# Kernel optimization log

Measured on AMD Instinct MI355X. Metric: run time of the kernel, lower is better.

Reference implementation:

```python
import jax, jax.numpy as jnp
import numpy as np

SEQ, BATCH = 1024, 2
N_HEAD, D_MODEL = 16, 1024
Q_LORA, KV_LORA = 20, 20
ROPE = D_MODEL // N_HEAD // 2   # 32 qk_rope_head_dim
NOPE = D_MODEL // N_HEAD // 2   # 32 qk_nope_head_dim
V_DIM = D_MODEL // N_HEAD       # 64
N_EXP, HID = 4, 1024            # hidden_dim = d_inner//5 = 5120//5
N_GROUP, TOPK_GROUP, TOP_K = 2, 2, 1
ROUTED_SCALE = 1.0


def setup_inputs() -> dict:
    key = jax.random.key(0)
    ks = jax.random.split(key, 16)
    sc = 0.02
    return {
        'dec_inp': jax.random.normal(ks[0], (SEQ, BATCH, D_MODEL), jnp.float32),
        'wq_a': jax.random.normal(ks[1], (D_MODEL, Q_LORA), jnp.float32) * sc,
        'q_norm_w': jnp.ones((Q_LORA,), jnp.float32),
        'wq_b': jax.random.normal(ks[2], (Q_LORA, N_HEAD * (NOPE + ROPE)), jnp.float32) * sc,
        'wkv_a': jax.random.normal(ks[3], (D_MODEL, KV_LORA + ROPE), jnp.float32) * sc,
        'kv_norm_w': jnp.ones((KV_LORA,), jnp.float32),
        'wkv_b': jax.random.normal(ks[4], (KV_LORA, N_HEAD * (NOPE + V_DIM)), jnp.float32) * sc,
        'wo': jax.random.normal(ks[5], (N_HEAD * V_DIM, D_MODEL), jnp.float32) * sc,
        'gate_w': jax.random.normal(ks[6], (N_EXP, D_MODEL), jnp.float32) * sc,
        'exp_gate': jax.random.normal(ks[7], (N_EXP, D_MODEL, HID), jnp.float32) * sc,
        'exp_up': jax.random.normal(ks[8], (N_EXP, D_MODEL, HID), jnp.float32) * sc,
        'exp_down': jax.random.normal(ks[9], (N_EXP, HID, D_MODEL), jnp.float32) * sc,
        'sh_gate': jax.random.normal(ks[10], (D_MODEL, HID), jnp.float32) * sc,
        'sh_up': jax.random.normal(ks[11], (D_MODEL, HID), jnp.float32) * sc,
        'sh_down': jax.random.normal(ks[12], (HID, D_MODEL), jnp.float32) * sc,
    }


def _rms(x, w, eps=1e-6):
    return x * jax.lax.rsqrt(jnp.mean(x * x, axis=-1, keepdims=True) + eps) * w


def _freqs(seqlen):
    # precompute_freqs_cis(rope_dim * n_head, seqlen): dim = 512 here
    dim = ROPE * N_HEAD
    inv = 1.0 / (10000.0 ** (jnp.arange(0, dim, 2, dtype=jnp.float32) / dim))  # [dim//2]
    ang = jnp.arange(seqlen, dtype=jnp.float32)[:, None] * inv[None, :]       # [s, dim//2]
    ang = ang.reshape(seqlen, N_HEAD, ROPE // 2)
    return jnp.cos(ang), jnp.sin(ang)


def _rope(x, cos, sin):
    # x: [b, s, h, ROPE]; interleaved-pair complex rotation
    b, s, h, _ = x.shape
    xr = x.reshape(b, s, h, ROPE // 2, 2)
    x0, x1 = xr[..., 0], xr[..., 1]
    c = cos[None]  # [1, s, h, ROPE//2]
    sn = sin[None]
    o0 = x0 * c - x1 * sn
    o1 = x0 * sn + x1 * c
    return jnp.stack([o0, o1], axis=-1).reshape(b, s, h, ROPE)


def reference(dec_inp, wq_a, q_norm_w, wq_b, wkv_a, kv_norm_w, wkv_b, wo,
              gate_w, exp_gate, exp_up, exp_down, sh_gate, sh_up, sh_down):
    x = jnp.swapaxes(dec_inp, 0, 1)  # [b, s, d]
    b, s, d = x.shape
    # ---- MLA attention ----
    q = _rms(x @ wq_a, q_norm_w) @ wq_b                       # [b, s, h*(nope+rope)]
    q = q.reshape(b, s, N_HEAD, NOPE + ROPE)
    q_nope, q_pe = q[..., :NOPE], q[..., NOPE:]
    kv = x @ wkv_a                                            # [b, s, kv_lora+rope]
    ckv, k_pe = kv[..., :KV_LORA], kv[..., KV_LORA:]
    kvb = (_rms(ckv, kv_norm_w) @ wkv_b).reshape(b, s, N_HEAD, NOPE + V_DIM)
    k_nope, v = kvb[..., :NOPE], kvb[..., NOPE:]
    cos, sin = _freqs(s)
    q_pe = _rope(q_pe, cos, sin)
    k_pe_h = _rope(jnp.broadcast_to(k_pe[:, :, None, :], (b, s, N_HEAD, ROPE)), cos, sin)
    qf = jnp.concatenate([q_nope, q_pe], axis=-1)             # [b, s, h, 64]
    kf = jnp.concatenate([k_nope, k_pe_h], axis=-1)
    scale = 1.0 / np.sqrt(NOPE + ROPE)
    scores = jnp.einsum('bshd,bthd->bhst', qf, kf) * scale    # mask=None in the source forward
    probs = jax.nn.softmax(scores, axis=-1)
    attn = jnp.einsum('bhst,bthd->bshd', probs, v).reshape(b, s, N_HEAD * V_DIM)
    y = attn @ wo                                             # [b, s, d]
    y = jnp.swapaxes(y, 0, 1)                                 # [s, b, d]
    # ---- DeepSeekMoE (group_limited_greedy, top_k=1, 1 shared expert) ----
    xf = y.reshape(-1, d)                                     # [T, d]
    T = xf.shape[0]
    sc = jax.nn.softmax(xf @ gate_w.T, axis=-1)               # [T, E]
    gsc = sc.reshape(T, N_GROUP, N_EXP // N_GROUP).max(axis=-1)  # [T, n_group]
    _, gidx = jax.lax.top_k(gsc, TOPK_GROUP)
    gmask = jax.nn.one_hot(gidx, N_GROUP, dtype=sc.dtype).sum(axis=1)  # [T, n_group]
    smask = jnp.repeat(gmask, N_EXP // N_GROUP, axis=-1)      # [T, E]
    tw, ti = jax.lax.top_k(jnp.where(smask > 0, sc, 0.0), TOP_K)
    comb = (jax.nn.one_hot(ti, N_EXP, dtype=sc.dtype) * tw[..., None]).sum(axis=1) * ROUTED_SCALE  # [T, E]
    g = jnp.einsum('td,edh->teh', xf, exp_gate)
    u = jnp.einsum('td,edh->teh', xf, exp_up)
    dn = jnp.einsum('teh,ehd->ted', jax.nn.silu(g) * u, exp_down)
    routed = jnp.einsum('ted,te->td', dn, comb)
    shared = (jax.nn.silu(xf @ sh_gate) * (xf @ sh_up)) @ sh_down
    return (routed + shared).reshape(s, b, d)
```

## Files before the change

### kernel.cpp

```cpp
#include <hip/hip_runtime.h>
#include <hip/hip_bf16.h>
#include <math.h>

#define SEQ 1024
#define BATCH 2
#define T 2048
#define DM 1024
#define NH 16
#define NOPE 32
#define HD 64
#define QL 20
#define KVL 20
#define KVA 52
#define HID 1024
#define NEXP 4
#define LSTR 80

typedef short bf16x8 __attribute__((ext_vector_type(8)));
typedef float f32x4 __attribute__((ext_vector_type(4)));
typedef float f32x16 __attribute__((ext_vector_type(16)));
typedef __hip_bfloat16 bf16;

static __device__ __forceinline__ float sigmoidf_(float x) {
    return 1.0f / (1.0f + __expf(-x));
}
static __device__ __forceinline__ unsigned short bfbits(float x) {
    bf16 h = __float2bfloat16(x);
    return *reinterpret_cast<unsigned short*>(&h);
}
static __device__ __forceinline__ unsigned cvt_pk_bf16(float lo, float hi) {
    unsigned r;
    asm("v_cvt_pk_bf16_f32 %0, %1, %2" : "=v"(r) : "v"(lo), "v"(hi));
    return r;
}
static __device__ __forceinline__ void gload16(const bf16* g, char* l) {
    __builtin_amdgcn_global_load_lds(
        (const __attribute__((address_space(1))) unsigned int*)g,
        (__attribute__((address_space(3))) unsigned int*)l, 16, 0, 0);
}
static __device__ __forceinline__ void barrier_() {
    asm volatile("" ::: "memory");
    __builtin_amdgcn_s_barrier();
    asm volatile("" ::: "memory");
}
#define VMWAIT(N) asm volatile("s_waitcnt vmcnt(" #N ")" ::: "memory")

__global__ __launch_bounds__(256) void k_setup(
    const float* __restrict__ wo, const float* __restrict__ sg,
    const float* __restrict__ su, const float* __restrict__ sd,
    const float* __restrict__ eg, const float* __restrict__ eu,
    const float* __restrict__ ed,
    bf16* __restrict__ woT, bf16* __restrict__ sgT, bf16* __restrict__ suT,
    bf16* __restrict__ sdT, bf16* __restrict__ egT, bf16* __restrict__ euT,
    bf16* __restrict__ edT,
    const float* __restrict__ wq_a, const float* __restrict__ wkv_a,
    const float* __restrict__ wq_b, const float* __restrict__ wkv_b,
    bf16* __restrict__ loraT, bf16* __restrict__ wqbT, bf16* __restrict__ wkvbT,
    float* __restrict__ ctab, float* __restrict__ stab)
{
    int z = blockIdx.z;
    int tid = threadIdx.x;
    if (z < 16) {
        __shared__ float tile[32][33];
        const float* in; bf16* out;
        if      (z == 0) { in = wo; out = woT; }
        else if (z == 1) { in = sg; out = sgT; }
        else if (z == 2) { in = su; out = suT; }
        else if (z == 3) { in = sd; out = sdT; }
        else if (z < 8)  { size_t o = (size_t)(z - 4)  * DM * HID; in = eg + o; out = egT + o; }
        else if (z < 12) { size_t o = (size_t)(z - 8)  * DM * HID; in = eu + o; out = euT + o; }
        else             { size_t o = (size_t)(z - 12) * HID * DM; in = ed + o; out = edT + o; }
        int c0 = blockIdx.x * 32, r0 = blockIdx.y * 32;
        int tx = tid & 31, ty = tid >> 5;
        #pragma unroll
        for (int ii = 0; ii < 4; ++ii)
            tile[ty + ii * 8][tx] = in[(size_t)(r0 + ty + ii * 8) * 1024 + c0 + tx];
        __syncthreads();
        int c = tid >> 3, rg = (tid & 7) * 4;
        ushort4 o4;
        o4.x = bfbits(tile[rg + 0][c]);
        o4.y = bfbits(tile[rg + 1][c]);
        o4.z = bfbits(tile[rg + 2][c]);
        o4.w = bfbits(tile[rg + 3][c]);
        *(ushort4*)&out[(size_t)(c0 + c) * 1024 + r0 + rg] = o4;
    } else if (z == 16) {
        int s = blockIdx.y * 32 + blockIdx.x;
        int p = tid;
        float freq = exp2f(-(float)p * (13.287712379549449f / 256.0f));
        float ang = (float)s * freq;
        float sn, cs;
        __sincosf(ang, &sn, &cs);
        ctab[s * 256 + p] = cs;
        stab[s * 256 + p] = sn;
    } else {
        int idx = (blockIdx.y * 32 + blockIdx.x) * 256 + tid;
        if (z == 17) {
            if (idx >= 80 * 1024) return;
            int n = idx >> 10, k = idx & 1023;
            float v = (n < 20) ? wq_a[k * QL + n] : (n < 72 ? wkv_a[k * KVA + (n - 20)] : 0.f);
            loraT[idx] = __float2bfloat16(v);
        } else if (z == 18) {
            if (idx >= 1024 * 32) return;
            int n = idx >> 5, k = idx & 31;
            wqbT[idx] = __float2bfloat16(k < 20 ? wq_b[k * DM + n] : 0.f);
        } else {
            if (idx >= 1536 * 32) return;
            int n = idx >> 5, k = idx & 31;
            wkvbT[idx] = __float2bfloat16(k < 20 ? wkv_b[k * (NH * 96) + n] : 0.f);
        }
    }
}

__global__ __launch_bounds__(256) void k_p1(
    const float* __restrict__ dec, const bf16* __restrict__ loraT,
    float* __restrict__ lora4)
{
    __shared__ __align__(16) char As[128 * LSTR];
    __shared__ __align__(16) char Bs[80 * LSTR];
    const int tid = threadIdx.x;
    const int kz = blockIdx.x;
    const int m0 = blockIdx.y * 128;
    const int lane = tid & 63, wave = tid >> 6;
    const int g = lane >> 4, c = lane & 15;
    f32x4 acc[2][5] = {};
    for (int ks = 0; ks < 16; ++ks) {
        int k0 = kz * 512 + ks * 32;
        __syncthreads();
        #pragma unroll
        for (int pass = 0; pass < 4; ++pass) {
            int row = (tid >> 3) + pass * 32;
            int t = m0 + row;
            int b = t >> 10, s = t & 1023;
            f32x4 v = *(const f32x4*)&dec[(size_t)(s * 2 + b) * DM + k0 + (tid & 7) * 4];
            ushort4 h4;
            h4.x = bfbits(v[0]); h4.y = bfbits(v[1]);
            h4.z = bfbits(v[2]); h4.w = bfbits(v[3]);
            *(ushort4*)&As[row * LSTR + (tid & 7) * 8] = h4;
        }
        if (tid < 160) {
            int row = tid >> 1, hf = tid & 1;
            const bf16* src = &loraT[row * 1024 + k0 + hf * 16];
            *(int4*)&Bs[row * LSTR + hf * 32]      = *(const int4*)&src[0];
            *(int4*)&Bs[row * LSTR + hf * 32 + 16] = *(const int4*)&src[8];
        }
        __syncthreads();
        bf16x8 af[2], bff[5];
        #pragma unroll
        for (int mi = 0; mi < 2; ++mi)
            af[mi] = *(const bf16x8*)&As[(wave * 32 + mi * 16 + c) * LSTR + 16 * g];
        #pragma unroll
        for (int nf = 0; nf < 5; ++nf)
            bff[nf] = *(const bf16x8*)&Bs[(nf * 16 + c) * LSTR + 16 * g];
        #pragma unroll
        for (int mi = 0; mi < 2; ++mi)
            #pragma unroll
            for (int nf = 0; nf < 5; ++nf)
                acc[mi][nf] = __builtin_amdgcn_mfma_f32_16x16x32_bf16(af[mi], bff[nf], acc[mi][nf], 0, 0, 0);
    }
    #pragma unroll
    for (int mi = 0; mi < 2; ++mi)
        #pragma unroll
        for (int nf = 0; nf < 5; ++nf)
            #pragma unroll
            for (int r = 0; r < 4; ++r) {
                int col = nf * 16 + c;
                if (col < 72) {
                    int row = m0 + wave * 32 + mi * 16 + 4 * g + r;
                    lora4[((size_t)kz * T + row) * 72 + col] = acc[mi][nf][r];
                }
            }
}

__global__ __launch_bounds__(256) void k_p2m(
    const float* __restrict__ lora4, const float* __restrict__ qnw,
    const float* __restrict__ kvnw, const float* __restrict__ ctab,
    const float* __restrict__ stab, bf16* __restrict__ nrmq,
    bf16* __restrict__ nrmkv, bf16* __restrict__ kb, int* __restrict__ cnt)
{
    int bid = blockIdx.x, tid = threadIdx.x;
    if (bid == 0 && tid < 16) cnt[tid] = 0;
    {
        int t = bid, p = tid;
        int r = p & 15, h = p >> 4, s = t & (SEQ - 1);
        float y0 = lora4[t * 72 + 40 + 2 * r] + lora4[(size_t)(T + t) * 72 + 40 + 2 * r];
        float y1 = lora4[t * 72 + 41 + 2 * r] + lora4[(size_t)(T + t) * 72 + 41 + 2 * r];
        float cs = ctab[s * 256 + p], sn = stab[s * 256 + p];
        ushort2 pk;
        pk.x = bfbits(y0 * cs - y1 * sn);
        pk.y = bfbits(y0 * sn + y1 * cs);
        *(ushort2*)&kb[(size_t)t * DM + h * HD + NOPE + 2 * r] = pk;
    }
    if (bid < 8) {
        int t = bid * 256 + tid;
        float lq[20], lk[20];
        float ssq = 0.f, ssk = 0.f;
        #pragma unroll
        for (int i = 0; i < 20; ++i) {
            lq[i] = lora4[t * 72 + i] + lora4[(size_t)(T + t) * 72 + i];
            ssq += lq[i] * lq[i];
        }
        #pragma unroll
        for (int i = 0; i < 20; ++i) {
            lk[i] = lora4[t * 72 + 20 + i] + lora4[(size_t)(T + t) * 72 + 20 + i];
            ssk += lk[i] * lk[i];
        }
        float fq = rsqrtf(ssq / 20.f + 1e-6f);
        float fk = rsqrtf(ssk / 20.f + 1e-6f);
        #pragma unroll
        for (int i = 0; i < 32; ++i) {
            nrmq[t * 32 + i]  = __float2bfloat16(i < 20 ? lq[i] * fq * qnw[i]  : 0.f);
            nrmkv[t * 32 + i] = __float2bfloat16(i < 20 ? lk[i] * fk * kvnw[i] : 0.f);
        }
    }
}

__global__ __launch_bounds__(256) void k_p3(
    const bf16* __restrict__ nrmq, const bf16* __restrict__ wqbT,
    const bf16* __restrict__ nrmkv, const bf16* __restrict__ wkvbT,
    const float* __restrict__ ctab, const float* __restrict__ stab,
    bf16* __restrict__ qb, bf16* __restrict__ kb, bf16* __restrict__ vt_g)
{
    const int zq = (blockIdx.z == 0);
    if (zq && blockIdx.x >= 16) return;
    __shared__ __align__(16) char As[128 * LSTR];
    __shared__ __align__(16) char Bs[64 * LSTR];
    const int tid = threadIdx.x;
    const int m0 = blockIdx.y * 128, n0 = blockIdx.x * 64;
    const int lane = tid & 63, wave = tid >> 6;
    const int g = lane >> 4, c = lane & 15;
    const int wm = wave >> 1, wn = wave & 1;
    const bf16* nrm = zq ? nrmq : nrmkv;
    const bf16* wT  = zq ? wqbT : wkvbT;
    {
        int row = tid >> 1, hf = tid & 1;
        const bf16* sa = &nrm[(size_t)(m0 + row) * 32 + hf * 16];
        *(int4*)&As[row * LSTR + hf * 32]      = *(const int4*)&sa[0];
        *(int4*)&As[row * LSTR + hf * 32 + 16] = *(const int4*)&sa[8];
        int brow = tid >> 2;
        *(int4*)&Bs[brow * LSTR + (tid & 3) * 16] = *(const int4*)&wT[(size_t)(n0 + brow) * 32 + (tid & 3) * 8];
    }
    __syncthreads();
    f32x4 acc[4][2] = {};
    bf16x8 af[4], bfr[2];
    #pragma unroll
    for (int mi = 0; mi < 4; ++mi)
        af[mi] = *(const bf16x8*)&As[(wm * 64 + mi * 16 + c) * LSTR + 16 * g];
    #pragma unroll
    for (int ni = 0; ni < 2; ++ni)
        bfr[ni] = *(const bf16x8*)&Bs[(wn * 32 + ni * 16 + c) * LSTR + 16 * g];
    #pragma unroll
    for (int mi = 0; mi < 4; ++mi)
        #pragma unroll
        for (int ni = 0; ni < 2; ++ni)
            acc[mi][ni] = __builtin_amdgcn_mfma_f32_16x16x32_bf16(af[mi], bfr[ni], acc[mi][ni], 0, 0, 0);

    if (zq) {
        #pragma unroll
        for (int mi = 0; mi < 4; ++mi)
            #pragma unroll
            for (int ni = 0; ni < 2; ++ni) {
                #pragma unroll
                for (int r = 0; r < 4; ++r) acc[mi][ni][r] *= 0.18033688f;
                int n = n0 + wn * 32 + ni * 16 + c;
                int w = n & 63;
                if (w < 32) {
                    #pragma unroll
                    for (int r = 0; r < 4; ++r) {
                        int row = m0 + wm * 64 + mi * 16 + 4 * g + r;
                        qb[(size_t)row * DM + n] = __float2bfloat16(acc[mi][ni][r]);
                    }
                } else {
                    int h = n >> 6;
                    int pidx = h * 16 + ((w - 32) >> 1);
                    int odd = w & 1;
                    #pragma unroll
                    for (int r = 0; r < 4; ++r) {
                        int row = m0 + wm * 64 + mi * 16 + 4 * g + r;
                        int s = row & (SEQ - 1);
                        float own = acc[mi][ni][r];
                        float oth = __shfl_xor(own, 1);
                        float cs = ctab[s * 256 + pidx], sn = stab[s * 256 + pidx];
                        float o = odd ? (oth * sn + own * cs) : (own * cs - oth * sn);
                        qb[(size_t)row * DM + n] = __float2bfloat16(o);
                    }
                }
            }
    } else {
        #pragma unroll
        for (int mi = 0; mi < 4; ++mi)
            #pragma unroll
            for (int ni = 0; ni < 2; ++ni) {
                int n = n0 + wn * 32 + ni * 16 + c;
                int h = n / 96, w = n - h * 96;
                int row0 = m0 + wm * 64 + mi * 16 + 4 * g;
                if (w < NOPE) {
                    #pragma unroll
                    for (int r = 0; r < 4; ++r)
                        kb[(size_t)(row0 + r) * DM + h * HD + w] = __float2bfloat16(acc[mi][ni][r]);
                } else {
                    int d = w - NOPE;
                    int b = row0 >> 10, s0 = row0 & (SEQ - 1);
                    ushort4 v4;
                    v4.x = bfbits(acc[mi][ni][0]);
                    v4.y = bfbits(acc[mi][ni][1]);
                    v4.z = bfbits(acc[mi][ni][2]);
                    v4.w = bfbits(acc[mi][ni][3]);
                    *(ushort4*)&vt_g[(((size_t)(b * NH + h) * HD + d) << 10) + s0] = v4;
                }
            }
    }
}

__global__ __launch_bounds__(256) void k_attn(
    const bf16* __restrict__ qb, const bf16* __restrict__ kb,
    const bf16* __restrict__ vt_g, bf16* __restrict__ ab)
{
    __shared__ __align__(16) char stage[2][16384];

    const int orig = blockIdx.y * 8 + blockIdx.x;
    const int h  = (orig & 7) * 2 + ((orig >> 3) & 1);
    const int qt = orig >> 4;
    const int b = blockIdx.z;
    const int tid = threadIdx.x;
    const int lane = tid & 63, wave = tid >> 6;
    const int l31 = lane & 31, hi = lane >> 5;
    const int sp = wave >> 1, wq = wave & 1;
    const int q0 = qt * 64 + wq * 32;
    char* ks = stage[sp];
    char* vt = stage[sp] + 8192;

    const int scol = ((lane & 7) * 8) ^ ((lane >> 3) << 3);
    const int srowL = lane >> 3;

    bf16x8 qf[4];
    {
        const bf16* qrow = &qb[(size_t)(b * SEQ + q0 + l31) * DM + h * HD + 8 * hi];
        #pragma unroll
        for (int st = 0; st < 4; ++st)
            qf[st] = *(const bf16x8*)&qrow[16 * st];
    }

    f32x16 o0 = {}, o1 = {};
    float m_run = -3.0e38f, l_run = 0.f;
    const size_t vbase = ((size_t)(b * NH + h) * HD) << 10;

    for (int ktl = 0; ktl < 8; ++ktl) {
        const int kt = sp * 8 + ktl;
        __syncthreads();
        #pragma unroll
        for (int ps = 0; ps < 4; ++ps) {
            int rbase = ps * 16 + wq * 8;
            int row = rbase + srowL;
            gload16(&kb[(size_t)(b * SEQ + kt * 64 + row) * DM + h * HD + scol],
                    ks + rbase * 128);
            gload16(&vt_g[vbase + ((size_t)row << 10) + kt * 64 + scol],
                    vt + rbase * 128);
        }
        VMWAIT(0);
        __syncthreads();

        f32x16 sc0 = {}, sc1 = {};
        __builtin_amdgcn_s_setprio(1);
        #pragma unroll
        for (int st = 0; st < 4; ++st) {
            int colb = 32 * st + 16 * hi;
            int r0 = l31;
            bf16x8 kf0 = *(const bf16x8*)&ks[r0 * 128 + (colb ^ ((r0 & 7) << 4))];
            sc0 = __builtin_amdgcn_mfma_f32_32x32x16_bf16(kf0, qf[st], sc0, 0, 0, 0);
            int r1 = 32 + l31;
            bf16x8 kf1 = *(const bf16x8*)&ks[r1 * 128 + (colb ^ ((r1 & 7) << 4))];
            sc1 = __builtin_amdgcn_mfma_f32_32x32x16_bf16(kf1, qf[st], sc1, 0, 0, 0);
        }
        __builtin_amdgcn_s_setprio(0);

        float mt = fmaxf(sc0[0], sc1[0]);
        #pragma unroll
        for (int i = 1; i < 16; ++i) mt = fmaxf(mt, fmaxf(sc0[i], sc1[i]));
        mt = fmaxf(mt, __shfl_xor(mt, 32));

        if (!__all(mt <= m_run + 8.0f)) {
            float m_new = fmaxf(m_run, mt);
            float corr = exp2f(m_run - m_new);
            m_run = m_new;
            l_run *= corr;
            #pragma unroll
            for (int i = 0; i < 16; ++i) { o0[i] *= corr; o1[i] *= corr; }
        }
        float ls = 0.f;
        #pragma unroll
        for (int i = 0; i < 16; ++i) {
            sc0[i] = exp2f(sc0[i] - m_run);
            sc1[i] = exp2f(sc1[i] - m_run);
            ls += sc0[i] + sc1[i];
        }
        ls += __shfl_xor(ls, 32);
        l_run += ls;

        unsigned pk0[8], pk1[8];
        #pragma unroll
        for (int i = 0; i < 8; ++i) {
            pk0[i] = cvt_pk_bf16(sc0[2 * i], sc0[2 * i + 1]);
            pk1[i] = cvt_pk_bf16(sc1[2 * i], sc1[2 * i + 1]);
        }

        __builtin_amdgcn_s_setprio(1);
#define PV_SUB(PK, KK)                                                          \
        {                                                                       \
            _Pragma("unroll")                                                   \
            for (int s = 0; s < 2; ++s) {                                       \
                unsigned sx = hi ? PK[4*s]   : PK[4*s+2];                       \
                unsigned rx = __shfl_xor(sx, 32);                               \
                unsigned sy = hi ? PK[4*s+1] : PK[4*s+3];                       \
                unsigned ry = __shfl_xor(sy, 32);                               \
                int4 bi;                                                        \
                bi.x = hi ? (int)rx : (int)PK[4*s];                             \
                bi.y = hi ? (int)ry : (int)PK[4*s+1];                           \
                bi.z = hi ? (int)PK[4*s+2] : (int)rx;                           \
                bi.w = hi ? (int)PK[4*s+3] : (int)ry;                           \
                bf16x8 bfr = *(bf16x8*)&bi;                                     \
                int cb = (KK) * 64 + 32 * s + 16 * hi;                          \
                {                                                               \
                    int vr = l31;                                               \
                    bf16x8 vf = *(const bf16x8*)&vt[vr * 128 + (cb ^ ((vr & 7) << 4))]; \
                    o0 = __builtin_amdgcn_mfma_f32_32x32x16_bf16(vf, bfr, o0, 0, 0, 0); \
                }                                                               \
                {                                                               \
                    int vr = 32 + l31;                                          \
                    bf16x8 vf = *(const bf16x8*)&vt[vr * 128 + (cb ^ ((vr & 7) << 4))]; \
                    o1 = __builtin_amdgcn_mfma_f32_32x32x16_bf16(vf, bfr, o1, 0, 0, 0); \
                }                                                               \
            }                                                                   \
        }
        PV_SUB(pk0, 0)
        PV_SUB(pk1, 1)
#undef PV_SUB
        __builtin_amdgcn_s_setprio(0);
    }

    float* polB = (float*)stage[0];
    float* mllB = (float*)(stage[0] + 16640 - 16384 + 16384);
    mllB = (float*)(stage[0] + 16640);

    __syncthreads();
    if (sp == 1) {
        #pragma unroll
        for (int i = 0; i < 16; ++i) {
            int d = (i & 3) + 8 * (i >> 2) + 4 * hi;
            polB[(wq * 32 + l31) * 65 + d]      = o0[i];
            polB[(wq * 32 + l31) * 65 + 32 + d] = o1[i];
        }
        if (hi == 0) {
            mllB[(wq * 32 + l31) * 2 + 0] = m_run;
            mllB[(wq * 32 + l31) * 2 + 1] = l_run;
        }
    }
    __syncthreads();
    if (sp == 0) {
        float m_b = mllB[(wq * 32 + l31) * 2 + 0];
        float l_b = mllB[(wq * 32 + l31) * 2 + 1];
        float M = fmaxf(m_run, m_b);
        float wa = exp2f(m_run - M), wb = exp2f(m_b - M);
        float inv = 1.0f / (l_run * wa + l_b * wb);
        #pragma unroll
        for (int i = 0; i < 16; ++i) {
            int d = (i & 3) + 8 * (i >> 2) + 4 * hi;
            o0[i] = (o0[i] * wa + polB[(wq * 32 + l31) * 65 + d]      * wb) * inv;
            o1[i] = (o1[i] * wa + polB[(wq * 32 + l31) * 65 + 32 + d] * wb) * inv;
        }
    }
    __syncthreads();
    if (sp == 0) {
        char* tb = stage[1] + 1024 + wq * 8192 / 2 * 0 + wq * 7168;
        tb = stage[1] + (wq ? 8192 : 1024);
        #pragma unroll
        for (int i = 0; i < 8; ++i) {
            int dbase = 2 * (i & 1) + 8 * (i >> 1) + 4 * hi;
            *(unsigned*)&tb[l31 * 140 + (dbase) * 2]      = cvt_pk_bf16(o0[2 * i], o0[2 * i + 1]);
            *(unsigned*)&tb[l31 * 140 + (32 + dbase) * 2] = cvt_pk_bf16(o1[2 * i], o1[2 * i + 1]);
        }
        __builtin_amdgcn_s_waitcnt(0);
        #pragma unroll
        for (int p = 0; p < 8; ++p) {
            int idx = p * 64 + lane;
            int q = idx >> 4, c8 = idx & 15;
            int2 rv;
            rv.x = *(const int*)&tb[q * 140 + c8 * 8];
            rv.y = *(const int*)&tb[q * 140 + c8 * 8 + 4];
            *(int2*)&ab[(size_t)(b * SEQ + q0 + q) * DM + h * HD + c8 * 4] = rv;
        }
    }
}

__global__ __launch_bounds__(512) void k_mm_plain(
    const bf16* __restrict__ A, const bf16* __restrict__ Bt, bf16* __restrict__ C)
{
    __shared__ __align__(16) char As[3][8192];
    __shared__ __align__(16) char Bs[3][4096];
    const int tid = threadIdx.x;
    const int lane = tid & 63, wave = tid >> 6;
    const int g = lane >> 4, c = lane & 15;
    const int wm = wave >> 1, wn = wave & 1;
    int orig = blockIdx.y * 16 + blockIdx.x;
    int swz = (orig & 7) * 32 + (orig >> 3);
    const int n0 = (swz & 15) * 64, m0 = (swz >> 4) * 128;

    const int ldr = lane >> 2;
    const int ldc = (lane & 3) * 8;
    const bf16* agp = &A[(size_t)(m0 + wave * 16 + ldr) * DM + ldc];
    const bool doB = wave >= 4;
    const bf16* bgp = &Bt[(size_t)(n0 + (wave & 3) * 16 + ldr) * DM + ldc];
    const int aoffL = wave * 1024, boffL = (wave & 3) * 1024;

    f32x4 acc[2][2] = {};
    const int NT = DM / 32;
    gload16(agp, As[0] + aoffL);
    if (doB) gload16(bgp, Bs[0] + boffL);
    int cur = 0;
    for (int k = 0; k < NT; ++k) {
        if (k + 1 < NT) {
            int nxt = (cur + 1) % 3;
            gload16(agp + (k + 1) * 32, As[nxt] + aoffL);
            if (doB) gload16(bgp + (k + 1) * 32, Bs[nxt] + boffL);
            if (doB) VMWAIT(2); else VMWAIT(1);
        } else {
            VMWAIT(0);
        }
        barrier_();
        bf16x8 af[2], bfx[2];
        #pragma unroll
        for (int mi = 0; mi < 2; ++mi)
            af[mi] = *(const bf16x8*)&As[cur][(wm * 32 + mi * 16 + c) * 64 + g * 16];
        #pragma unroll
        for (int ni = 0; ni < 2; ++ni)
            bfx[ni] = *(const bf16x8*)&Bs[cur][(wn * 32 + ni * 16 + c) * 64 + g * 16];
        #pragma unroll
        for (int mi = 0; mi < 2; ++mi)
            #pragma unroll
            for (int ni = 0; ni < 2; ++ni)
                acc[mi][ni] = __builtin_amdgcn_mfma_f32_16x16x32_bf16(af[mi], bfx[ni], acc[mi][ni], 0, 0, 0);
        cur = (cur + 1) % 3;
    }
    #pragma unroll
    for (int mi = 0; mi < 2; ++mi)
        #pragma unroll
        for (int ni = 0; ni < 2; ++ni)
            #pragma unroll
            for (int r = 0; r < 4; ++r)
                C[(size_t)(m0 + wm * 32 + mi * 16 + 4 * g + r) * DM + n0 + wn * 32 + ni * 16 + c]
                    = __float2bfloat16(acc[mi][ni][r]);
}

__global__ __launch_bounds__(512) void k_mm_gu_all(
    const bf16* __restrict__ X, const bf16* __restrict__ egT,
    const bf16* __restrict__ euT, const bf16* __restrict__ sgT,
    const bf16* __restrict__ suT, const int* __restrict__ cnt,
    const int* __restrict__ lists, bf16* __restrict__ act_r,
    bf16* __restrict__ act_s)
{
    const int e = blockIdx.z;
    const bool SH = (e == 4);
    const int ntok = SH ? T : cnt[e];
    int orig = blockIdx.y * 16 + blockIdx.x;
    int swz = (orig & 7) * 32 + (orig >> 3);
    const int n0 = (swz & 15) * 64, m0 = (swz >> 4) * 128;
    if (m0 >= ntok) return;
    __shared__ __align__(16) char As[3][8192];
    __shared__ __align__(16) char Bg[3][4096];
    __shared__ __align__(16) char Bu[3][4096];
    __shared__ int rowid[128];
    const int tid = threadIdx.x;
    if (tid < 128) {
        int idx = m0 + tid;
        rowid[tid] = SH ? idx : lists[e * T + (idx < ntok ? idx : ntok - 1)];
    }
    __syncthreads();
    const int lane = tid & 63, wave = tid >> 6;
    const int g = lane >> 4, c = lane & 15;
    const int wm = wave >> 1, wn = wave & 1;
    const bf16* Bge = SH ? sgT : egT + (size_t)e * HID * DM;
    const bf16* Bue = SH ? suT : euT + (size_t)e * HID * DM;
    bf16* act = SH ? act_s : act_r;

    const int ldr = lane >> 2;
    const int ldc = (lane & 3) * 8;
    const int myTok = rowid[wave * 16 + ldr];
    const bf16* agp = &X[(size_t)myTok * DM + ldc];
    const bool isG = wave < 4;
    const bf16* bgp = (isG ? Bge : Bue) + (size_t)(n0 + (wave & 3) * 16 + ldr) * DM + ldc;
    const int aoffL = wave * 1024, boffL = (wave & 3) * 1024;

    f32x4 accg[2][2] = {}, accu[2][2] = {};
    const int NT = DM / 32;
    gload16(agp, As[0] + aoffL);
    gload16(bgp, (isG ? Bg[0] : Bu[0]) + boffL);
    int cur = 0;
    for (int k = 0; k < NT; ++k) {
        if (k + 1 < NT) {
            int nxt = (cur + 1) % 3;
            gload16(agp + (k + 1) * 32, As[nxt] + aoffL);
            gload16(bgp + (k + 1) * 32, (isG ? Bg[nxt] : Bu[nxt]) + boffL);
            VMWAIT(2);
        } else {
            VMWAIT(0);
        }
        barrier_();
        bf16x8 af[2], gf[2], uf[2];
        #pragma unroll
        for (int mi = 0; mi < 2; ++mi)
            af[mi] = *(const bf16x8*)&As[cur][(wm * 32 + mi * 16 + c) * 64 + g * 16];
        #pragma unroll
        for (int ni = 0; ni < 2; ++ni) {
            gf[ni] = *(const bf16x8*)&Bg[cur][(wn * 32 + ni * 16 + c) * 64 + g * 16];
            uf[ni] = *(const bf16x8*)&Bu[cur][(wn * 32 + ni * 16 + c) * 64 + g * 16];
        }
        #pragma unroll
        for (int mi = 0; mi < 2; ++mi)
            #pragma unroll
            for (int ni = 0; ni < 2; ++ni) {
                accg[mi][ni] = __builtin_amdgcn_mfma_f32_16x16x32_bf16(af[mi], gf[ni], accg[mi][ni], 0, 0, 0);
                accu[mi][ni] = __builtin_amdgcn_mfma_f32_16x16x32_bf16(af[mi], uf[ni], accu[mi][ni], 0, 0, 0);
            }
        cur = (cur + 1) % 3;
    }
    #pragma unroll
    for (int mi = 0; mi < 2; ++mi)
        #pragma unroll
        for (int ni = 0; ni < 2; ++ni)
            #pragma unroll
            for (int r = 0; r < 4; ++r) {
                int lr = wm * 32 + mi * 16 + 4 * g + r;
                if (!SH && m0 + lr >= ntok) continue;
                int token = rowid[lr];
                float gv = accg[mi][ni][r], uv = accu[mi][ni][r];
                act[(size_t)token * HID + n0 + wn * 32 + ni * 16 + c] =
                    __float2bfloat16(gv * sigmoidf_(gv) * uv);
            }
}

__global__ __launch_bounds__(512) void k_mm_down_f(
    const bf16* __restrict__ Xr, const bf16* __restrict__ Xs,
    const bf16* __restrict__ edT, const bf16* __restrict__ sdT,
    const int* __restrict__ cnt, const int* __restrict__ lists,
    const float* __restrict__ wtok, float* __restrict__ out)
{
    const int e = blockIdx.z;
    const int ntok = cnt[e];
    int orig = blockIdx.y * 16 + blockIdx.x;
    int swz = (orig & 7) * 32 + (orig >> 3);
    const int n0 = (swz & 15) * 64, m0 = (swz >> 4) * 128;
    if (m0 >= ntok) return;
    __shared__ __align__(16) char Ar[3][8192];
    __shared__ __align__(16) char Az[3][8192];
    __shared__ __align__(16) char Br[3][4096];
    __shared__ __align__(16) char Bz[3][4096];
    __shared__ int rowid[128];
    const int tid = threadIdx.x;
    if (tid < 128) {
        int idx = m0 + tid;
        rowid[tid] = lists[e * T + (idx < ntok ? idx : ntok - 1)];
    }
    __syncthreads();
    const int lane = tid & 63, wave = tid >> 6;
    const int g = lane >> 4, c = lane & 15;
    const int wm = wave >> 1, wn = wave & 1;
    const bf16* Bde = edT + (size_t)e * HID * DM;

    const int ldr = lane >> 2;
    const int ldc = (lane & 3) * 8;
    const int myTok = rowid[wave * 16 + ldr];
    const bf16* agr = &Xr[(size_t)myTok * HID + ldc];
    const bf16* ags = &Xs[(size_t)myTok * HID + ldc];
    const bool isR = wave < 4;
    const bf16* bgp = (isR ? Bde : sdT) + (size_t)(n0 + (wave & 3) * 16 + ldr) * HID + ldc;
    const int aoffL = wave * 1024, boffL = (wave & 3) * 1024;

    f32x4 accr[2][2] = {}, accs[2][2] = {};
    const int NT = HID / 32;
    gload16(agr, Ar[0] + aoffL);
    gload16(ags, Az[0] + aoffL);
    gload16(bgp, (isR ? Br[0] : Bz[0]) + boffL);
    int cur = 0;
    for (int k = 0; k < NT; ++k) {
        if (k + 1 < NT) {
            int nxt = (cur + 1) % 3;
            gload16(agr + (k + 1) * 32, Ar[nxt] + aoffL);
            gload16(ags + (k + 1) * 32, Az[nxt] + aoffL);
            gload16(bgp + (k + 1) * 32, (isR ? Br[nxt] : Bz[nxt]) + boffL);
            VMWAIT(3);
        } else {
            VMWAIT(0);
        }
        barrier_();
        bf16x8 afr[2], afs[2], bfr[2], bfs[2];
        #pragma unroll
        for (int mi = 0; mi < 2; ++mi) {
            afr[mi] = *(const bf16x8*)&Ar[cur][(wm * 32 + mi * 16 + c) * 64 + g * 16];
            afs[mi] = *(const bf16x8*)&Az[cur][(wm * 32 + mi * 16 + c) * 64 + g * 16];
        }
        #pragma unroll
        for (int ni = 0; ni < 2; ++ni) {
            bfr[ni] = *(const bf16x8*)&Br[cur][(wn * 32 + ni * 16 + c) * 64 + g * 16];
            bfs[ni] = *(const bf16x8*)&Bz[cur][(wn * 32 + ni * 16 + c) * 64 + g * 16];
        }
        #pragma unroll
        for (int mi = 0; mi < 2; ++mi)
            #pragma unroll
            for (int ni = 0; ni < 2; ++ni) {
                accr[mi][ni] = __builtin_amdgcn_mfma_f32_16x16x32_bf16(afr[mi], bfr[ni], accr[mi][ni], 0, 0, 0);
                accs[mi][ni] = __builtin_amdgcn_mfma_f32_16x16x32_bf16(afs[mi], bfs[ni], accs[mi][ni], 0, 0, 0);
            }
        cur = (cur + 1) % 3;
    }
    #pragma unroll
    for (int mi = 0; mi < 2; ++mi)
        #pragma unroll
        for (int ni = 0; ni < 2; ++ni)
            #pragma unroll
            for (int r = 0; r < 4; ++r) {
                int lr = wm * 32 + mi * 16 + 4 * g + r;
                if (m0 + lr >= ntok) continue;
                int token = rowid[lr];
                int bt = token >> 10, st = token & (SEQ - 1);
                size_t oo = (size_t)st * (BATCH * DM) + bt * DM + n0 + wn * 32 + ni * 16 + c;
                out[oo] = accr[mi][ni][r] * wtok[token] + accs[mi][ni][r];
            }
}

__global__ __launch_bounds__(256) void k_gate(
    const bf16* __restrict__ y, const float* __restrict__ gw,
    int* __restrict__ cnt, int* __restrict__ lists, float* __restrict__ wtok)
{
    int warp = threadIdx.x >> 6, lane = threadIdx.x & 63;
    int t = blockIdx.x * 4 + warp;
    float acc[NEXP] = {};
    for (int d = lane; d < DM; d += 64) {
        float xv = __bfloat162float(y[(size_t)t * DM + d]);
        #pragma unroll
        for (int e = 0; e < NEXP; ++e) acc[e] += xv * gw[e * DM + d];
    }
    #pragma unroll
    for (int off = 32; off; off >>= 1)
        #pragma unroll
        for (int e = 0; e < NEXP; ++e) acc[e] += __shfl_xor(acc[e], off);
    if (lane == 0) {
        float mx = fmaxf(fmaxf(acc[0], acc[1]), fmaxf(acc[2], acc[3]));
        float ex[NEXP], ssum = 0.f;
        #pragma unroll
        for (int e = 0; e < NEXP; ++e) { ex[e] = __expf(acc[e] - mx); ssum += ex[e]; }
        int best = 0; float bv = ex[0];
        #pragma unroll
        for (int e = 1; e < NEXP; ++e) if (ex[e] > bv) { bv = ex[e]; best = e; }
        wtok[t] = bv / ssum;
        int pos = atomicAdd(&cnt[best], 1);
        lists[best * T + pos] = t;
    }
}

extern "C" void kernel_launch(void* const* d_in, const int* in_sizes, int n_in,
                              void* d_out, int out_size, void* d_ws, size_t ws_size,
                              hipStream_t stream) {
    (void)in_sizes; (void)n_in; (void)out_size; (void)ws_size;
    const float* dec      = (const float*)d_in[0];
    const float* wq_a     = (const float*)d_in[1];
    const float* q_norm_w = (const float*)d_in[2];
    const float* wq_b     = (const float*)d_in[3];
    const float* wkv_a    = (const float*)d_in[4];
    const float* kv_norm_w= (const float*)d_in[5];
    const float* wkv_b    = (const float*)d_in[6];
    const float* wo       = (const float*)d_in[7];
    const float* gate_w   = (const float*)d_in[8];
    const float* exp_gate = (const float*)d_in[9];
    const float* exp_up   = (const float*)d_in[10];
    const float* exp_down = (const float*)d_in[11];
    const float* sh_gate  = (const float*)d_in[12];
    const float* sh_up    = (const float*)d_in[13];
    const float* sh_down  = (const float*)d_in[14];
    float* out = (float*)d_out;

    char* W = (char*)d_ws;
    bf16* qb   = (bf16*)(W);
    bf16* kb   = (bf16*)(W + (4ull  << 20));
    bf16* vt_g = (bf16*)(W + (8ull  << 20));
    char* SMALL = W + (12ull << 20);
    bf16* ab   = (bf16*)(W + (12ull << 20));
    bf16* woT = (bf16*)(W + (16ull << 20));
    bf16* sgT = (bf16*)(W + (18ull << 20));
    bf16* suT = (bf16*)(W + (20ull << 20));
    bf16* sdT = (bf16*)(W + (22ull << 20));
    bf16* egT = (bf16*)(W + (24ull << 20));
    bf16* euT = (bf16*)(W + (32ull << 20));
    bf16* edT = (bf16*)(W + (40ull << 20));
    int*   cnt   = (int*)(W + (48ull << 20));
    int*   lists = cnt + 16;
    float* wtok  = (float*)(lists + NEXP * T);
    bf16* yb    = qb;
    bf16* act_r = kb;
    bf16* act_s = vt_g;

    float* lora4 = (float*)(SMALL);
    bf16*  loraT = (bf16*) (SMALL + 1179648);
    bf16*  wqbT  = (bf16*) (SMALL + 1343488);
    bf16*  wkvbT = (bf16*) (SMALL + 1409024);
    bf16*  nrmq  = (bf16*) (SMALL + 1507328);
    bf16*  nrmkv = (bf16*) (SMALL + 1638400);
    float* ctab  = (float*)(SMALL + 1769472);
    float* stab  = (float*)(SMALL + 2818048);

    k_setup<<<dim3(32, 32, 20), 256, 0, stream>>>(
        wo, sh_gate, sh_up, sh_down, exp_gate, exp_up, exp_down,
        woT, sgT, suT, sdT, egT, euT, edT,
        wq_a, wkv_a, wq_b, wkv_b, loraT, wqbT, wkvbT, ctab, stab);

    k_p1<<<dim3(2, 16), 256, 0, stream>>>(dec, loraT, lora4);
    k_p2m<<<T, 256, 0, stream>>>(lora4, q_norm_w, kv_norm_w, ctab, stab,
                                 nrmq, nrmkv, kb, cnt);
    k_p3<<<dim3(24, 16, 2), 256, 0, stream>>>(nrmq, wqbT, nrmkv, wkvbT,
                                              ctab, stab, qb, kb, vt_g);

    k_attn<<<dim3(8, 32, BATCH), 256, 0, stream>>>(qb, kb, vt_g, ab);
    k_mm_plain<<<dim3(16, 16), 512, 0, stream>>>(ab, woT, yb);
    k_gate<<<T / 4, 256, 0, stream>>>(yb, gate_w, cnt, lists, wtok);
    k_mm_gu_all<<<dim3(16, 16, NEXP + 1), 512, 0, stream>>>(
        yb, egT, euT, sgT, suT, cnt, lists, act_r, act_s);
    k_mm_down_f<<<dim3(16, 16, NEXP), 512, 0, stream>>>(
        act_r, act_s, edT, sdT, cnt, lists, wtok, out);
}
```

Before: 172.5 us.

## Fuse FFN weight transpose/bf16 conversion into MoE GEMM B-tile loads

Drops the setup pass that transposed and converted all expert and shared FFN weights to bf16. The gate/up and down GEMM kernels now load fp32 weights directly into registers, convert them to bf16 and write them transposed into LDS, with a two-stage prefetch and LGKM wait plus barrier. This removes a large extra read and write of about 60MB of weights per call. In exchange, the main GEMM loops read fp32 (twice the bytes) through ordinary loads and do scalar 2-byte LDS stores.

```diff
diff --git a/kernel.cpp b/kernel.cpp
--- a/kernel.cpp
+++ b/kernel.cpp
@@ -44,15 +44,10 @@
     asm volatile("" ::: "memory");
 }
 #define VMWAIT(N) asm volatile("s_waitcnt vmcnt(" #N ")" ::: "memory")
+#define LGKM0()   asm volatile("s_waitcnt lgkmcnt(0)" ::: "memory")
 
 __global__ __launch_bounds__(256) void k_setup(
-    const float* __restrict__ wo, const float* __restrict__ sg,
-    const float* __restrict__ su, const float* __restrict__ sd,
-    const float* __restrict__ eg, const float* __restrict__ eu,
-    const float* __restrict__ ed,
-    bf16* __restrict__ woT, bf16* __restrict__ sgT, bf16* __restrict__ suT,
-    bf16* __restrict__ sdT, bf16* __restrict__ egT, bf16* __restrict__ euT,
-    bf16* __restrict__ edT,
+    const float* __restrict__ wo, bf16* __restrict__ woT,
     const float* __restrict__ wq_a, const float* __restrict__ wkv_a,
     const float* __restrict__ wq_b, const float* __restrict__ wkv_b,
     bf16* __restrict__ loraT, bf16* __restrict__ wqbT, bf16* __restrict__ wkvbT,
@@ -60,21 +55,13 @@
 {
     int z = blockIdx.z;
     int tid = threadIdx.x;
-    if (z < 16) {
+    if (z == 0) {
         __shared__ float tile[32][33];
-        const float* in; bf16* out;
-        if      (z == 0) { in = wo; out = woT; }
-        else if (z == 1) { in = sg; out = sgT; }
-        else if (z == 2) { in = su; out = suT; }
-        else if (z == 3) { in = sd; out = sdT; }
-        else if (z < 8)  { size_t o = (size_t)(z - 4)  * DM * HID; in = eg + o; out = egT + o; }
-        else if (z < 12) { size_t o = (size_t)(z - 8)  * DM * HID; in = eu + o; out = euT + o; }
-        else             { size_t o = (size_t)(z - 12) * HID * DM; in = ed + o; out = edT + o; }
         int c0 = blockIdx.x * 32, r0 = blockIdx.y * 32;
         int tx = tid & 31, ty = tid >> 5;
         #pragma unroll
         for (int ii = 0; ii < 4; ++ii)
-            tile[ty + ii * 8][tx] = in[(size_t)(r0 + ty + ii * 8) * 1024 + c0 + tx];
+            tile[ty + ii * 8][tx] = wo[(size_t)(r0 + ty + ii * 8) * 1024 + c0 + tx];
         __syncthreads();
         int c = tid >> 3, rg = (tid & 7) * 4;
         ushort4 o4;
@@ -82,8 +69,8 @@
         o4.y = bfbits(tile[rg + 1][c]);
         o4.z = bfbits(tile[rg + 2][c]);
         o4.w = bfbits(tile[rg + 3][c]);
-        *(ushort4*)&out[(size_t)(c0 + c) * 1024 + r0 + rg] = o4;
-    } else if (z == 16) {
+        *(ushort4*)&woT[(size_t)(c0 + c) * 1024 + r0 + rg] = o4;
+    } else if (z == 1) {
         int s = blockIdx.y * 32 + blockIdx.x;
         int p = tid;
         float freq = exp2f(-(float)p * (13.287712379549449f / 256.0f));
@@ -94,12 +81,12 @@
         stab[s * 256 + p] = sn;
     } else {
         int idx = (blockIdx.y * 32 + blockIdx.x) * 256 + tid;
-        if (z == 17) {
+        if (z == 2) {
             if (idx >= 80 * 1024) return;
             int n = idx >> 10, k = idx & 1023;
             float v = (n < 20) ? wq_a[k * QL + n] : (n < 72 ? wkv_a[k * KVA + (n - 20)] : 0.f);
             loraT[idx] = __float2bfloat16(v);
-        } else if (z == 18) {
+        } else if (z == 3) {
             if (idx >= 1024 * 32) return;
             int n = idx >> 5, k = idx & 31;
             wqbT[idx] = __float2bfloat16(k < 20 ? wq_b[k * DM + n] : 0.f);
@@ -438,8 +425,7 @@
     }
 
     float* polB = (float*)stage[0];
-    float* mllB = (float*)(stage[0] + 16640 - 16384 + 16384);
-    mllB = (float*)(stage[0] + 16640);
+    float* mllB = (float*)(stage[0] + 16640);
 
     __syncthreads();
     if (sp == 1) {
@@ -470,8 +456,7 @@
     }
     __syncthreads();
     if (sp == 0) {
-        char* tb = stage[1] + 1024 + wq * 8192 / 2 * 0 + wq * 7168;
-        tb = stage[1] + (wq ? 8192 : 1024);
+        char* tb = stage[1] + (wq ? 8192 : 1024);
         #pragma unroll
         for (int i = 0; i < 8; ++i) {
             int dbase = 2 * (i & 1) + 8 * (i >> 1) + 4 * hi;
@@ -551,9 +536,9 @@
 }
 
 __global__ __launch_bounds__(512) void k_mm_gu_all(
-    const bf16* __restrict__ X, const bf16* __restrict__ egT,
-    const bf16* __restrict__ euT, const bf16* __restrict__ sgT,
-    const bf16* __restrict__ suT, const int* __restrict__ cnt,
+    const bf16* __restrict__ X, const float* __restrict__ eg,
+    const float* __restrict__ eu, const float* __restrict__ sg,
+    const float* __restrict__ su, const int* __restrict__ cnt,
     const int* __restrict__ lists, bf16* __restrict__ act_r,
     bf16* __restrict__ act_s)
 {
@@ -577,8 +562,8 @@
     const int lane = tid & 63, wave = tid >> 6;
     const int g = lane >> 4, c = lane & 15;
     const int wm = wave >> 1, wn = wave & 1;
-    const bf16* Bge = SH ? sgT : egT + (size_t)e * HID * DM;
-    const bf16* Bue = SH ? suT : euT + (size_t)e * HID * DM;
+    const float* Wg = SH ? sg : eg + (size_t)e * DM * HID;
+    const float* Wu = SH ? su : eu + (size_t)e * DM * HID;
     bf16* act = SH ? act_s : act_r;
 
     const int ldr = lane >> 2;
@@ -586,24 +571,48 @@
     const int myTok = rowid[wave * 16 + ldr];
     const bf16* agp = &X[(size_t)myTok * DM + ldc];
     const bool isG = wave < 4;
-    const bf16* bgp = (isG ? Bge : Bue) + (size_t)(n0 + (wave & 3) * 16 + ldr) * DM + ldc;
-    const int aoffL = wave * 1024, boffL = (wave & 3) * 1024;
-
+    const int w4 = wave & 3, nb0 = w4 * 16;
+    const int ng = lane & 3, kk = lane >> 2;
+    const float* bq = (isG ? Wg : Wu) + (size_t)kk * HID + n0 + nb0 + ng * 4;
+    const int aoffL = wave * 1024;
+
+#define BWRITE(BUF)                                                             \
+    {                                                                           \
+        char* bb = (isG ? Bg[BUF] : Bu[BUF]);                                   \
+        _Pragma("unroll")                                                       \
+        for (int j = 0; j < 4; ++j) {                                           \
+            *(unsigned short*)&bb[(nb0 + ng * 4 + j) * 64 + kk * 2]        = bfbits(b0[j]); \
+            *(unsigned short*)&bb[(nb0 + ng * 4 + j) * 64 + (kk + 16) * 2] = bfbits(b1[j]); \
+        }                                                                       \
+    }
+
+    f32x4 b0, b1;
     f32x4 accg[2][2] = {}, accu[2][2] = {};
     const int NT = DM / 32;
+    b0 = *(const f32x4*)(bq);
+    b1 = *(const f32x4*)(bq + 16 * HID);
     gload16(agp, As[0] + aoffL);
-    gload16(bgp, (isG ? Bg[0] : Bu[0]) + boffL);
+    VMWAIT(1);
+    BWRITE(0)
+    b0 = *(const f32x4*)(bq + 32 * HID);
+    b1 = *(const f32x4*)(bq + 48 * HID);
+    gload16(agp + 32, As[1] + aoffL);
+    LGKM0();
+    barrier_();
     int cur = 0;
     for (int k = 0; k < NT; ++k) {
         if (k + 1 < NT) {
             int nxt = (cur + 1) % 3;
-            gload16(agp + (k + 1) * 32, As[nxt] + aoffL);
-            gload16(bgp + (k + 1) * 32, (isG ? Bg[nxt] : Bu[nxt]) + boffL);
-            VMWAIT(2);
+            VMWAIT(1);
+            BWRITE(nxt)
+            if (k + 2 < NT) {
+                b0 = *(const f32x4*)(bq + (size_t)(k + 2) * 32 * HID);
+                b1 = *(const f32x4*)(bq + (size_t)(k + 2) * 32 * HID + 16 * HID);
+                gload16(agp + (k + 2) * 32, As[(nxt + 1) % 3] + aoffL);
+            }
         } else {
             VMWAIT(0);
         }
-        barrier_();
         bf16x8 af[2], gf[2], uf[2];
         #pragma unroll
         for (int mi = 0; mi < 2; ++mi)
@@ -620,8 +629,11 @@
                 accg[mi][ni] = __builtin_amdgcn_mfma_f32_16x16x32_bf16(af[mi], gf[ni], accg[mi][ni], 0, 0, 0);
                 accu[mi][ni] = __builtin_amdgcn_mfma_f32_16x16x32_bf16(af[mi], uf[ni], accu[mi][ni], 0, 0, 0);
             }
+        LGKM0();
+        barrier_();
         cur = (cur + 1) % 3;
     }
+#undef BWRITE
     #pragma unroll
     for (int mi = 0; mi < 2; ++mi)
         #pragma unroll
@@ -639,7 +651,7 @@
 
 __global__ __launch_bounds__(512) void k_mm_down_f(
     const bf16* __restrict__ Xr, const bf16* __restrict__ Xs,
-    const bf16* __restrict__ edT, const bf16* __restrict__ sdT,
+    const float* __restrict__ ed, const float* __restrict__ sd,
     const int* __restrict__ cnt, const int* __restrict__ lists,
     const float* __restrict__ wtok, float* __restrict__ out)
 {
@@ -663,7 +675,6 @@
     const int lane = tid & 63, wave = tid >> 6;
     const int g = lane >> 4, c = lane & 15;
     const int wm = wave >> 1, wn = wave & 1;
-    const bf16* Bde = edT + (size_t)e * HID * DM;
 
     const int ldr = lane >> 2;
     const int ldc = (lane & 3) * 8;
@@ -671,26 +682,52 @@
     const bf16* agr = &Xr[(size_t)myTok * HID + ldc];
     const bf16* ags = &Xs[(size_t)myTok * HID + ldc];
     const bool isR = wave < 4;
-    const bf16* bgp = (isR ? Bde : sdT) + (size_t)(n0 + (wave & 3) * 16 + ldr) * HID + ldc;
-    const int aoffL = wave * 1024, boffL = (wave & 3) * 1024;
-
+    const int w4 = wave & 3, nb0 = w4 * 16;
+    const int ng = lane & 3, kk = lane >> 2;
+    const float* bq = (isR ? (ed + (size_t)e * HID * DM) : sd)
+                      + (size_t)kk * DM + n0 + nb0 + ng * 4;
+    const int aoffL = wave * 1024;
+
+#define BWRITE(BUF)                                                             \
+    {                                                                           \
+        char* bb = (isR ? Br[BUF] : Bz[BUF]);                                   \
+        _Pragma("unroll")                                                       \
+        for (int j = 0; j < 4; ++j) {                                           \
+            *(unsigned short*)&bb[(nb0 + ng * 4 + j) * 64 + kk * 2]        = bfbits(b0[j]); \
+            *(unsigned short*)&bb[(nb0 + ng * 4 + j) * 64 + (kk + 16) * 2] = bfbits(b1[j]); \
+        }                                                                       \
+    }
+
+    f32x4 b0, b1;
     f32x4 accr[2][2] = {}, accs[2][2] = {};
     const int NT = HID / 32;
+    b0 = *(const f32x4*)(bq);
+    b1 = *(const f32x4*)(bq + 16 * DM);
     gload16(agr, Ar[0] + aoffL);
     gload16(ags, Az[0] + aoffL);
-    gload16(bgp, (isR ? Br[0] : Bz[0]) + boffL);
+    VMWAIT(2);
+    BWRITE(0)
+    b0 = *(const f32x4*)(bq + 32 * DM);
+    b1 = *(const f32x4*)(bq + 48 * DM);
+    gload16(agr + 32, Ar[1] + aoffL);
+    gload16(ags + 32, Az[1] + aoffL);
+    LGKM0();
+    barrier_();
     int cur = 0;
     for (int k = 0; k < NT; ++k) {
         if (k + 1 < NT) {
             int nxt = (cur + 1) % 3;
-            gload16(agr + (k + 1) * 32, Ar[nxt] + aoffL);
-            gload16(ags + (k + 1) * 32, Az[nxt] + aoffL);
-            gload16(bgp + (k + 1) * 32, (isR ? Br[nxt] : Bz[nxt]) + boffL);
-            VMWAIT(3);
+            VMWAIT(2);
+            BWRITE(nxt)
+            if (k + 2 < NT) {
+                b0 = *(const f32x4*)(bq + (size_t)(k + 2) * 32 * DM);
+                b1 = *(const f32x4*)(bq + (size_t)(k + 2) * 32 * DM + 16 * DM);
+                gload16(agr + (k + 2) * 32, Ar[(nxt + 1) % 3] + aoffL);
+                gload16(ags + (k + 2) * 32, Az[(nxt + 1) % 3] + aoffL);
+            }
         } else {
             VMWAIT(0);
         }
-        barrier_();
         bf16x8 afr[2], afs[2], bfr[2], bfs[2];
         #pragma unroll
         for (int mi = 0; mi < 2; ++mi) {
@@ -709,8 +746,11 @@
                 accr[mi][ni] = __builtin_amdgcn_mfma_f32_16x16x32_bf16(afr[mi], bfr[ni], accr[mi][ni], 0, 0, 0);
                 accs[mi][ni] = __builtin_amdgcn_mfma_f32_16x16x32_bf16(afs[mi], bfs[ni], accs[mi][ni], 0, 0, 0);
             }
+        LGKM0();
+        barrier_();
         cur = (cur + 1) % 3;
     }
+#undef BWRITE
     #pragma unroll
     for (int mi = 0; mi < 2; ++mi)
         #pragma unroll
@@ -783,13 +823,7 @@
     bf16* vt_g = (bf16*)(W + (8ull  << 20));
     char* SMALL = W + (12ull << 20);
     bf16* ab   = (bf16*)(W + (12ull << 20));
-    bf16* woT = (bf16*)(W + (16ull << 20));
-    bf16* sgT = (bf16*)(W + (18ull << 20));
-    bf16* suT = (bf16*)(W + (20ull << 20));
-    bf16* sdT = (bf16*)(W + (22ull << 20));
-    bf16* egT = (bf16*)(W + (24ull << 20));
-    bf16* euT = (bf16*)(W + (32ull << 20));
-    bf16* edT = (bf16*)(W + (40ull << 20));
+    bf16* woT  = (bf16*)(W + (16ull << 20));
     int*   cnt   = (int*)(W + (48ull << 20));
     int*   lists = cnt + 16;
     float* wtok  = (float*)(lists + NEXP * T);
@@ -806,10 +840,8 @@
     float* ctab  = (float*)(SMALL + 1769472);
     float* stab  = (float*)(SMALL + 2818048);
 
-    k_setup<<<dim3(32, 32, 20), 256, 0, stream>>>(
-        wo, sh_gate, sh_up, sh_down, exp_gate, exp_up, exp_down,
-        woT, sgT, suT, sdT, egT, euT, edT,
-        wq_a, wkv_a, wq_b, wkv_b, loraT, wqbT, wkvbT, ctab, stab);
+    k_setup<<<dim3(32, 32, 5), 256, 0, stream>>>(
+        wo, woT, wq_a, wkv_a, wq_b, wkv_b, loraT, wqbT, wkvbT, ctab, stab);
 
     k_p1<<<dim3(2, 16), 256, 0, stream>>>(dec, loraT, lora4);
     k_p2m<<<T, 256, 0, stream>>>(lora4, q_norm_w, kv_norm_w, ctab, stab,
@@ -821,7 +853,7 @@
     k_mm_plain<<<dim3(16, 16), 512, 0, stream>>>(ab, woT, yb);
     k_gate<<<T / 4, 256, 0, stream>>>(yb, gate_w, cnt, lists, wtok);
     k_mm_gu_all<<<dim3(16, 16, NEXP + 1), 512, 0, stream>>>(
-        yb, egT, euT, sgT, suT, cnt, lists, act_r, act_s);
+        yb, exp_gate, exp_up, sh_gate, sh_up, cnt, lists, act_r, act_s);
     k_mm_down_f<<<dim3(16, 16, NEXP), 512, 0, stream>>>(
-        act_r, act_s, edT, sdT, cnt, lists, wtok, out);
-}
+        act_r, act_s, exp_down, sh_down, cnt, lists, wtok, out);
+}
```

Result: slower. 201.2 us (+16.6%).
